# Optimization experiments

Hardware: AMD Instinct MI355X
Metric: run time of the kernel (lower is better)

The kernel has to match this reference:

```python
import jax, jax.numpy as jnp
import numpy as np

B, S, E, H = 2, 2048, 1024, 16
D = E // H  # head_dim = 64


def setup_inputs() -> dict:
    key = jax.random.key(0)
    ks = jax.random.split(key, 6)
    sc = 1.0 / np.sqrt(D)
    return {
        "x": jax.random.normal(ks[0], (B, S, E), dtype=jnp.float32),
        "Wq": jax.random.normal(ks[1], (D, D), dtype=jnp.float32) * sc,
        "Wk": jax.random.normal(ks[2], (D, D), dtype=jnp.float32) * sc,
        "Wv": jax.random.normal(ks[3], (D, D), dtype=jnp.float32) * sc,
        "Wo": jax.random.normal(ks[4], (E, E), dtype=jnp.float32) * (1.0 / np.sqrt(E)),
        "bo": jnp.zeros((E,), dtype=jnp.float32),
    }


def reference(x, Wq, Wk, Wv, Wo, bo):
    b, s, e = x.shape
    # split into heads: (B, H, S, D)
    xh = x.reshape(b, s, H, D).transpose(0, 2, 1, 3)
    # per-head linear projections (weights SHARED across heads); torch Linear: x @ W^T
    q = jnp.einsum('bhsd,ed->bhse', xh, Wq)
    k = jnp.einsum('bhsd,ed->bhse', xh, Wk)
    v = jnp.einsum('bhsd,ed->bhse', xh, Wv)
    # full attention matrix (B, H, S, S) — faithful to the naive original
    energy = jnp.einsum('bhqd,bhkd->bhqk', q, k)
    attn = jax.nn.softmax(energy / jnp.sqrt(jnp.asarray(D, x.dtype)), axis=-1)
    out = jnp.einsum('bhqk,bhkd->bhqd', attn, v)
    out = out.transpose(0, 2, 1, 3).reshape(b, s, e)
    return out @ Wo.T + bo
```

## Files before the change

### kernel.cpp

```cpp
#include <hip/hip_runtime.h>
#include <hip/hip_bf16.h>

#define B 2
#define S 2048
#define E 1024
#define H 16
#define D 64

typedef unsigned short ushort_t;
typedef __attribute__((ext_vector_type(8))) short bf16x8;
typedef __attribute__((ext_vector_type(4))) float f32x4;
typedef __attribute__((ext_vector_type(16))) float f32x16;

static __device__ __forceinline__ ushort_t f2bf(float f) {
    union { float f; unsigned u; } v; v.f = f;
    unsigned r = v.u + 0x7fffu + ((v.u >> 16) & 1u);
    return (ushort_t)(r >> 16);
}

#define MFMA(a, b, c)   __builtin_amdgcn_mfma_f32_16x16x32_bf16((a), (b), (c), 0, 0, 0)
#define MFMA32(a, b, c) __builtin_amdgcn_mfma_f32_32x32x16_bf16((a), (b), (c), 0, 0, 0)
#define PACKBF(hi, lo) __builtin_amdgcn_perm((hi), (lo), 0x07060302u)
#define LBAR() do { asm volatile("s_waitcnt lgkmcnt(0)" ::: "memory"); \
                    __builtin_amdgcn_s_barrier(); } while (0)

__global__ __launch_bounds__(256) void qkv_proj(
    const float* __restrict__ x,
    const float* __restrict__ Wq, const float* __restrict__ Wk, const float* __restrict__ Wv,
    const float* __restrict__ Wo,
    ushort_t* __restrict__ q, ushort_t* __restrict__ k, ushort_t* __restrict__ vT,
    ushort_t* __restrict__ wob)
{
    __shared__ ushort_t Xs[64][72];
    __shared__ ushort_t Wqs[64][72], Wks[64][72], Wvs[64][72];
    int t = threadIdx.x;
    int bh = blockIdx.y, b = bh >> 4, h = bh & 15;
    int s0 = blockIdx.x * 64;

    {
        int woid = blockIdx.y * 32 + blockIdx.x;
        int i = woid * 1024 + t * 4;
        float4 f = *(const float4*)(Wo + i);
        ushort4 u2; u2.x = f2bf(f.x); u2.y = f2bf(f.y); u2.z = f2bf(f.z); u2.w = f2bf(f.w);
        *(ushort4*)(wob + i) = u2;
    }
    {
        int i = t >> 2, d0 = (t & 3) * 16;
        const float* xp = x + ((size_t)(b * S + s0 + i)) * E + h * D + d0;
        #pragma unroll
        for (int c = 0; c < 16; c += 4) {
            float4 f = *(const float4*)(xp + c);
            Xs[i][d0 + c + 0] = f2bf(f.x); Xs[i][d0 + c + 1] = f2bf(f.y);
            Xs[i][d0 + c + 2] = f2bf(f.z); Xs[i][d0 + c + 3] = f2bf(f.w);
        }
    }
    {
        int e = t >> 2, d0 = (t & 3) * 16;
        const float* wqp = Wq + e * 64 + d0;
        const float* wkp = Wk + e * 64 + d0;
        const float* wvp = Wv + e * 64 + d0;
        #pragma unroll
        for (int c = 0; c < 16; c += 4) {
            float4 fq = *(const float4*)(wqp + c);
            Wqs[e][d0 + c + 0] = f2bf(fq.x * 0.18033688011112042f);
            Wqs[e][d0 + c + 1] = f2bf(fq.y * 0.18033688011112042f);
            Wqs[e][d0 + c + 2] = f2bf(fq.z * 0.18033688011112042f);
            Wqs[e][d0 + c + 3] = f2bf(fq.w * 0.18033688011112042f);
            float4 fk = *(const float4*)(wkp + c);
            Wks[e][d0 + c + 0] = f2bf(fk.x); Wks[e][d0 + c + 1] = f2bf(fk.y);
            Wks[e][d0 + c + 2] = f2bf(fk.z); Wks[e][d0 + c + 3] = f2bf(fk.w);
            float4 fv = *(const float4*)(wvp + c);
            Wvs[e][d0 + c + 0] = f2bf(fv.x); Wvs[e][d0 + c + 1] = f2bf(fv.y);
            Wvs[e][d0 + c + 2] = f2bf(fv.z); Wvs[e][d0 + c + 3] = f2bf(fv.w);
        }
    }
    __syncthreads();

    int w = t >> 6, lane = t & 63, m = lane & 15, quad = lane >> 4;
    bf16x8 a0 = *(bf16x8*)&Xs[16 * w + m][quad * 8];
    bf16x8 a1 = *(bf16x8*)&Xs[16 * w + m][32 + quad * 8];
    f32x4 cq[4], ck[4], cv[4];
    #pragma unroll
    for (int nt = 0; nt < 4; nt++) { cq[nt] = (f32x4)0.f; ck[nt] = (f32x4)0.f; cv[nt] = (f32x4)0.f; }
    #pragma unroll
    for (int nt = 0; nt < 4; nt++) {
        bf16x8 b0, b1;
        b0 = *(bf16x8*)&Wqs[nt * 16 + m][quad * 8]; b1 = *(bf16x8*)&Wqs[nt * 16 + m][32 + quad * 8];
        cq[nt] = MFMA(a0, b0, cq[nt]); cq[nt] = MFMA(a1, b1, cq[nt]);
        b0 = *(bf16x8*)&Wks[nt * 16 + m][quad * 8]; b1 = *(bf16x8*)&Wks[nt * 16 + m][32 + quad * 8];
        ck[nt] = MFMA(a0, b0, ck[nt]); ck[nt] = MFMA(a1, b1, ck[nt]);
        b0 = *(bf16x8*)&Wvs[nt * 16 + m][quad * 8]; b1 = *(bf16x8*)&Wvs[nt * 16 + m][32 + quad * 8];
        cv[nt] = MFMA(a0, b0, cv[nt]); cv[nt] = MFMA(a1, b1, cv[nt]);
    }
    size_t base = (size_t)bh * S + s0;
    #pragma unroll
    for (int nt = 0; nt < 4; nt++)
        #pragma unroll
        for (int r = 0; r < 4; r++) {
            size_t idx = (base + 16 * w + quad * 4 + r) * D + nt * 16 + m;
            q[idx] = f2bf(cq[nt][r]);
            k[idx] = f2bf(ck[nt][r]);
        }
    __syncthreads();
    #pragma unroll
    for (int nt = 0; nt < 4; nt++)
        #pragma unroll
        for (int r = 0; r < 4; r++)
            Wvs[nt * 16 + m][16 * w + quad * 4 + r] = f2bf(cv[nt][r]);
    __syncthreads();
    {
        int d0 = t >> 2, sc = (t & 3) * 16;
        ushort_t* vp = vT + ((size_t)bh * D + d0) * S + s0 + sc;
        *(bf16x8*)(vp)     = *(bf16x8*)&Wvs[d0][sc];
        *(bf16x8*)(vp + 8) = *(bf16x8*)&Wvs[d0][sc + 8];
    }
}

__global__ __launch_bounds__(512, 4) void flash_attn(
    const ushort_t* __restrict__ q, const ushort_t* __restrict__ k,
    const ushort_t* __restrict__ vT, ushort_t* __restrict__ ao)
{
    __shared__ ushort_t Ks[2][2][64][72];
    __shared__ ushort_t Vt[2][2][64][72];
    int t = threadIdx.x;
    int lin = blockIdx.x;
    int xcd = lin & 7, loc = lin >> 3;
    int bh = xcd * 4 + (loc >> 4);
    int q0 = (loc & 15) * 128;
    int b = bh >> 4, h = bh & 15;
    int w = t >> 6, lane = t & 63, l31 = lane & 31, half = lane >> 5;
    int g = w >> 2, wq = w & 3;
    int tg = t & 255;

    const ushort_t* qb = q + ((size_t)bh * S + q0) * D;
    const ushort_t* kb = k + (size_t)bh * S * D;
    const ushort_t* vb = vT + (size_t)bh * D * S;

    bf16x8 qf[4];
    {
        const ushort_t* qp = qb + (size_t)(wq * 32 + l31) * D + half * 8;
        #pragma unroll
        for (int c = 0; c < 4; c++) qf[c] = *(const bf16x8*)(qp + c * 16);
    }

    f32x16 o0 = (f32x16)0.f, o1 = (f32x16)0.f;
    float2 ls2 = make_float2(0.f, 0.f);

    int sr = tg >> 2, scc = (tg & 3) * 16;
    bf16x8 kp0, kp1, vp0, vp1;

    {
        int k00 = g * 64;
        const ushort_t* kp = kb + (size_t)(k00 + sr) * D + scc;
        const ushort_t* vp = vb + (size_t)sr * S + k00 + scc;
        kp0 = *(const bf16x8*)(kp);     kp1 = *(const bf16x8*)(kp + 8);
        vp0 = *(const bf16x8*)(vp);     vp1 = *(const bf16x8*)(vp + 8);
        *(bf16x8*)&Ks[g][0][sr][scc]     = kp0;
        *(bf16x8*)&Ks[g][0][sr][scc + 8] = kp1;
        *(bf16x8*)&Vt[g][0][sr][scc]     = vp0;
        *(bf16x8*)&Vt[g][0][sr][scc + 8] = vp1;
    }
    LBAR();
    {
        int k01 = (2 + g) * 64;
        const ushort_t* kp = kb + (size_t)(k01 + sr) * D + scc;
        const ushort_t* vp = vb + (size_t)sr * S + k01 + scc;
        kp0 = *(const bf16x8*)(kp);     kp1 = *(const bf16x8*)(kp + 8);
        vp0 = *(const bf16x8*)(vp);     vp1 = *(const bf16x8*)(vp + 8);
    }

    const int NJ = S / 128;
    for (int jt = 0; jt < NJ; jt++) {
        int p = jt & 1;
        if (jt + 1 < NJ) {
            *(bf16x8*)&Ks[g][1 - p][sr][scc]     = kp0;
            *(bf16x8*)&Ks[g][1 - p][sr][scc + 8] = kp1;
            *(bf16x8*)&Vt[g][1 - p][sr][scc]     = vp0;
            *(bf16x8*)&Vt[g][1 - p][sr][scc + 8] = vp1;
        }
        if (jt + 2 < NJ) {
            int k0n = (2 * (jt + 2) + g) * 64;
            const ushort_t* kp = kb + (size_t)(k0n + sr) * D + scc;
            const ushort_t* vp = vb + (size_t)sr * S + k0n + scc;
            kp0 = *(const bf16x8*)(kp);     kp1 = *(const bf16x8*)(kp + 8);
            vp0 = *(const bf16x8*)(vp);     vp1 = *(const bf16x8*)(vp + 8);
        }

        union { unsigned u[4]; bf16x8 v; } pa[4];
        #pragma unroll
        for (int st = 0; st < 2; st++) {
            f32x16 e = (f32x16)0.f;
            __builtin_amdgcn_s_setprio(1);
            #pragma unroll
            for (int c = 0; c < 4; c++) {
                bf16x8 ka = *(bf16x8*)&Ks[g][p][st * 32 + l31][c * 16 + half * 8];
                e = MFMA32(ka, qf[c], e);
            }
            __builtin_amdgcn_s_setprio(0);
            unsigned pt[16];
            #pragma unroll
            for (int r = 0; r < 16; r += 2) {
                float pe0 = __builtin_amdgcn_exp2f(e[r]);
                float pe1 = __builtin_amdgcn_exp2f(e[r + 1]);
                ls2.x += pe0; ls2.y += pe1;
                pt[r]     = __float_as_uint(pe0);
                pt[r + 1] = __float_as_uint(pe1);
            }
            #pragma unroll
            for (int c2 = 0; c2 < 2; c2++) {
                int rb = c2 * 8;
                unsigned dA = PACKBF(pt[rb + 1], pt[rb + 0]);
                unsigned dB = PACKBF(pt[rb + 3], pt[rb + 2]);
                unsigned dC = PACKBF(pt[rb + 5], pt[rb + 4]);
                unsigned dD = PACKBF(pt[rb + 7], pt[rb + 6]);
                asm volatile("v_permlane32_swap_b32 %0, %1" : "+v"(dA), "+v"(dC));
                asm volatile("v_permlane32_swap_b32 %0, %1" : "+v"(dB), "+v"(dD));
                int kc = st * 2 + c2;
                pa[kc].u[0] = dA;
                pa[kc].u[1] = dB;
                pa[kc].u[2] = dC;
                pa[kc].u[3] = dD;
            }
        }

        __builtin_amdgcn_s_setprio(1);
        #pragma unroll
        for (int kc = 0; kc < 4; kc++) {
            bf16x8 vf0 = *(bf16x8*)&Vt[g][p][l31][kc * 16 + half * 8];
            bf16x8 vf1 = *(bf16x8*)&Vt[g][p][32 + l31][kc * 16 + half * 8];
            o0 = MFMA32(pa[kc].v, vf0, o0);
            o1 = MFMA32(pa[kc].v, vf1, o1);
        }
        __builtin_amdgcn_s_setprio(0);
        LBAR();
    }

    float lsum = ls2.x + ls2.y;
    float* cmb = (float*)&Ks[0][0][0][0];
    int slot = (wq * 64 + lane) * 33;
    if (g == 1) {
        #pragma unroll
        for (int r2 = 0; r2 < 16; r2++) { cmb[slot + r2] = o0[r2]; cmb[slot + 16 + r2] = o1[r2]; }
        cmb[slot + 32] = lsum;
    }
    __syncthreads();
    if (g == 0) {
        #pragma unroll
        for (int r2 = 0; r2 < 16; r2++) { o0[r2] += cmb[slot + r2]; o1[r2] += cmb[slot + 16 + r2]; }
        lsum += cmb[slot + 32];
        float lfull = lsum + __shfl_xor(lsum, 32, 64);
        float inv = 1.001953125f / lfull;
        #pragma unroll
        for (int reg = 0; reg < 16; reg++) {
            int qrow = (reg & 3) + 8 * (reg >> 2) + 4 * half;
            float li = __shfl(inv, qrow, 64);
            int srow = q0 + wq * 32 + qrow;
            size_t base2 = ((size_t)(b * S + srow)) * E + h * D + l31;
            ao[base2]      = f2bf(o0[reg] * li);
            ao[base2 + 32] = f2bf(o1[reg] * li);
        }
    }
}

__global__ __launch_bounds__(512) void out_proj(
    const ushort_t* __restrict__ A, const ushort_t* __restrict__ Wob,
    const float* __restrict__ bo, float* __restrict__ Y)
{
    __shared__ ushort_t As[2][128][72];
    __shared__ ushort_t Ws[2][64][72];
    int t = threadIdx.x;
    int hwb = blockIdx.x;
    int swz = (hwb & 7) * 64 + (hwb >> 3);
    int n0 = (swz & 15) * 64, m0 = (swz >> 4) * 128;
    int w = t >> 6, lane = t & 63, m = lane & 15, quad = lane >> 4;
    f32x4 acc[4];
    #pragma unroll
    for (int nt = 0; nt < 4; nt++) acc[nt] = (f32x4)0.f;

    int ar = t >> 2, ac = (t & 3) * 16;
    int wr = t >> 3, wc = (t & 7) * 8;
    const ushort_t* apb = A + (size_t)(m0 + ar) * E + ac;
    const ushort_t* wpb = Wob + (size_t)(n0 + wr) * E + wc;

    bf16x8 arg[2], wrg;
    {
        *(bf16x8*)&As[0][ar][ac]     = *(const bf16x8*)(apb);
        *(bf16x8*)&As[0][ar][ac + 8] = *(const bf16x8*)(apb + 8);
        *(bf16x8*)&Ws[0][wr][wc]     = *(const bf16x8*)(wpb);
    }
    LBAR();
    {
        arg[0] = *(const bf16x8*)(apb + 64);
        arg[1] = *(const bf16x8*)(apb + 64 + 8);
        wrg    = *(const bf16x8*)(wpb + 64);
    }

    const int KT = E / 64;
    for (int ks = 0; ks < KT; ks++) {
        int p = ks & 1;
        if (ks + 1 < KT) {
            *(bf16x8*)&As[1 - p][ar][ac]     = arg[0];
            *(bf16x8*)&As[1 - p][ar][ac + 8] = arg[1];
            *(bf16x8*)&Ws[1 - p][wr][wc]     = wrg;
        }
        if (ks + 2 < KT) {
            int off = (ks + 2) * 64;
            arg[0] = *(const bf16x8*)(apb + off);
            arg[1] = *(const bf16x8*)(apb + off + 8);
            wrg    = *(const bf16x8*)(wpb + off);
        }
        #pragma unroll
        for (int h2 = 0; h2 < 2; h2++) {
            bf16x8 af = *(bf16x8*)&As[p][w * 16 + m][h2 * 32 + quad * 8];
            #pragma unroll
            for (int nt = 0; nt < 4; nt++) {
                bf16x8 bfr = *(bf16x8*)&Ws[p][nt * 16 + m][h2 * 32 + quad * 8];
                acc[nt] = MFMA(af, bfr, acc[nt]);
            }
        }
        LBAR();
    }
    #pragma unroll
    for (int nt = 0; nt < 4; nt++)
        #pragma unroll
        for (int r = 0; r < 4; r++) {
            int row = m0 + w * 16 + quad * 4 + r;
            int col = n0 + nt * 16 + m;
            Y[(size_t)row * E + col] = acc[nt][r] + bo[col];
        }
}

extern "C" void kernel_launch(void* const* d_in, const int* in_sizes, int n_in,
                              void* d_out, int out_size, void* d_ws, size_t ws_size,
                              hipStream_t stream)
{
    const float* x  = (const float*)d_in[0];
    const float* Wq = (const float*)d_in[1];
    const float* Wk = (const float*)d_in[2];
    const float* Wv = (const float*)d_in[3];
    const float* Wo = (const float*)d_in[4];
    const float* bo = (const float*)d_in[5];
    float* Y = (float*)d_out;

    const size_t n = (size_t)B * H * S * D;
    ushort_t* qw  = (ushort_t*)d_ws;
    ushort_t* kw  = qw + n;
    ushort_t* vTw = kw + n;
    ushort_t* ao  = vTw + n;
    ushort_t* wob = ao + n;

    qkv_proj<<<dim3(S / 64, B * H), 256, 0, stream>>>(x, Wq, Wk, Wv, Wo, qw, kw, vTw, wob);
    flash_attn<<<dim3((S / 128) * B * H), 512, 0, stream>>>(qw, kw, vTw, ao);
    out_proj<<<dim3(512), 512, 0, stream>>>(ao, wob, bo, Y);
}
```

Baseline: 141.8 us.

## Fuse projection, attention and output GEMM into one cooperative kernel with grid syncs

Merges the three kernels (QKV projection, flash attention, output projection) into a single cooperative persistent kernel of 512 blocks. The phases are separated by grid.sync and reuse one shared-memory buffer. The aim is to remove the launch gaps and tails between kernels. In exchange, the QKV phase now uses 512-thread blocks, each covering two 64-row halves, and the kernel depends on every block being co-resident (512 blocks at 4 per CU). If the cooperative launch fails, it falls back to the original three launches.

```diff
diff --git a/kernel.cpp b/kernel.cpp
--- a/kernel.cpp
+++ b/kernel.cpp
@@ -1,5 +1,8 @@
 #include <hip/hip_runtime.h>
 #include <hip/hip_bf16.h>
+#include <hip/hip_cooperative_groups.h>
+
+namespace cg = cooperative_groups;
 
 #define B 2
 #define S 2048
@@ -21,8 +24,317 @@
 #define MFMA(a, b, c)   __builtin_amdgcn_mfma_f32_16x16x32_bf16((a), (b), (c), 0, 0, 0)
 #define MFMA32(a, b, c) __builtin_amdgcn_mfma_f32_32x32x16_bf16((a), (b), (c), 0, 0, 0)
 #define PACKBF(hi, lo) __builtin_amdgcn_perm((hi), (lo), 0x07060302u)
+#define WQSCALE 0.18033688011112042f
 #define LBAR() do { asm volatile("s_waitcnt lgkmcnt(0)" ::: "memory"); \
                     __builtin_amdgcn_s_barrier(); } while (0)
+
+__global__ __launch_bounds__(512, 4) void fused_all(
+    const float* __restrict__ x,
+    const float* __restrict__ Wq, const float* __restrict__ Wk, const float* __restrict__ Wv,
+    const float* __restrict__ Wo, const float* __restrict__ bo,
+    ushort_t* __restrict__ q, ushort_t* __restrict__ k, ushort_t* __restrict__ vT,
+    ushort_t* __restrict__ ao, ushort_t* __restrict__ wob, float* __restrict__ Y)
+{
+    __shared__ char smem[73728];
+    cg::grid_group grid = cg::this_grid();
+    int th = threadIdx.x;
+    int lin = blockIdx.x;
+    int xcd = lin & 7, loc = lin >> 3;
+    int bh = xcd * 4 + (loc >> 4);
+    int b = bh >> 4, h = bh & 15;
+
+    {
+        ushort_t (*Xs)[64][72] = (ushort_t (*)[64][72])smem;
+        ushort_t (*Wqs)[72] = (ushort_t (*)[72])(smem + 18432);
+        ushort_t (*Wks)[72] = (ushort_t (*)[72])(smem + 27648);
+        ushort_t (*Wvs)[72] = (ushort_t (*)[72])(smem + 36864);
+        int hhalf = th >> 8, t = th & 255;
+        int s0 = (loc & 15) * 128 + hhalf * 64;
+
+        {
+            int i = lin * 2048 + th * 4;
+            float4 f = *(const float4*)(Wo + i);
+            ushort4 u2; u2.x = f2bf(f.x); u2.y = f2bf(f.y); u2.z = f2bf(f.z); u2.w = f2bf(f.w);
+            *(ushort4*)(wob + i) = u2;
+        }
+        {
+            int i = t >> 2, d0 = (t & 3) * 16;
+            const float* xp = x + ((size_t)(b * S + s0 + i)) * E + h * D + d0;
+            #pragma unroll
+            for (int c = 0; c < 16; c += 4) {
+                float4 f = *(const float4*)(xp + c);
+                Xs[hhalf][i][d0 + c + 0] = f2bf(f.x); Xs[hhalf][i][d0 + c + 1] = f2bf(f.y);
+                Xs[hhalf][i][d0 + c + 2] = f2bf(f.z); Xs[hhalf][i][d0 + c + 3] = f2bf(f.w);
+            }
+        }
+        {
+            int rw = th >> 3, c8 = (th & 7) * 8;
+            const float* wqp = Wq + rw * 64 + c8;
+            const float* wkp = Wk + rw * 64 + c8;
+            const float* wvp = Wv + rw * 64 + c8;
+            float4 f0 = *(const float4*)(wqp), f1 = *(const float4*)(wqp + 4);
+            Wqs[rw][c8 + 0] = f2bf(f0.x * WQSCALE); Wqs[rw][c8 + 1] = f2bf(f0.y * WQSCALE);
+            Wqs[rw][c8 + 2] = f2bf(f0.z * WQSCALE); Wqs[rw][c8 + 3] = f2bf(f0.w * WQSCALE);
+            Wqs[rw][c8 + 4] = f2bf(f1.x * WQSCALE); Wqs[rw][c8 + 5] = f2bf(f1.y * WQSCALE);
+            Wqs[rw][c8 + 6] = f2bf(f1.z * WQSCALE); Wqs[rw][c8 + 7] = f2bf(f1.w * WQSCALE);
+            f0 = *(const float4*)(wkp); f1 = *(const float4*)(wkp + 4);
+            Wks[rw][c8 + 0] = f2bf(f0.x); Wks[rw][c8 + 1] = f2bf(f0.y);
+            Wks[rw][c8 + 2] = f2bf(f0.z); Wks[rw][c8 + 3] = f2bf(f0.w);
+            Wks[rw][c8 + 4] = f2bf(f1.x); Wks[rw][c8 + 5] = f2bf(f1.y);
+            Wks[rw][c8 + 6] = f2bf(f1.z); Wks[rw][c8 + 7] = f2bf(f1.w);
+            f0 = *(const float4*)(wvp); f1 = *(const float4*)(wvp + 4);
+            Wvs[rw][c8 + 0] = f2bf(f0.x); Wvs[rw][c8 + 1] = f2bf(f0.y);
+            Wvs[rw][c8 + 2] = f2bf(f0.z); Wvs[rw][c8 + 3] = f2bf(f0.w);
+            Wvs[rw][c8 + 4] = f2bf(f1.x); Wvs[rw][c8 + 5] = f2bf(f1.y);
+            Wvs[rw][c8 + 6] = f2bf(f1.z); Wvs[rw][c8 + 7] = f2bf(f1.w);
+        }
+        __syncthreads();
+
+        int w = (th >> 6) & 3, lane = th & 63, m = lane & 15, quad = lane >> 4;
+        bf16x8 a0 = *(bf16x8*)&Xs[hhalf][16 * w + m][quad * 8];
+        bf16x8 a1 = *(bf16x8*)&Xs[hhalf][16 * w + m][32 + quad * 8];
+        f32x4 cq[4], ck[4], cv[4];
+        #pragma unroll
+        for (int nt = 0; nt < 4; nt++) { cq[nt] = (f32x4)0.f; ck[nt] = (f32x4)0.f; cv[nt] = (f32x4)0.f; }
+        #pragma unroll
+        for (int nt = 0; nt < 4; nt++) {
+            bf16x8 b0, b1;
+            b0 = *(bf16x8*)&Wqs[nt * 16 + m][quad * 8]; b1 = *(bf16x8*)&Wqs[nt * 16 + m][32 + quad * 8];
+            cq[nt] = MFMA(a0, b0, cq[nt]); cq[nt] = MFMA(a1, b1, cq[nt]);
+            b0 = *(bf16x8*)&Wks[nt * 16 + m][quad * 8]; b1 = *(bf16x8*)&Wks[nt * 16 + m][32 + quad * 8];
+            ck[nt] = MFMA(a0, b0, ck[nt]); ck[nt] = MFMA(a1, b1, ck[nt]);
+            b0 = *(bf16x8*)&Wvs[nt * 16 + m][quad * 8]; b1 = *(bf16x8*)&Wvs[nt * 16 + m][32 + quad * 8];
+            cv[nt] = MFMA(a0, b0, cv[nt]); cv[nt] = MFMA(a1, b1, cv[nt]);
+        }
+        size_t base = (size_t)bh * S + s0;
+        #pragma unroll
+        for (int nt = 0; nt < 4; nt++)
+            #pragma unroll
+            for (int r = 0; r < 4; r++) {
+                size_t idx = (base + 16 * w + quad * 4 + r) * D + nt * 16 + m;
+                q[idx] = f2bf(cq[nt][r]);
+                k[idx] = f2bf(ck[nt][r]);
+            }
+        __syncthreads();
+        #pragma unroll
+        for (int nt = 0; nt < 4; nt++)
+            #pragma unroll
+            for (int r = 0; r < 4; r++)
+                Xs[hhalf][nt * 16 + m][16 * w + quad * 4 + r] = f2bf(cv[nt][r]);
+        __syncthreads();
+        {
+            int d0 = t >> 2, sc = (t & 3) * 16;
+            ushort_t* vp = vT + ((size_t)bh * D + d0) * S + s0 + sc;
+            *(bf16x8*)(vp)     = *(bf16x8*)&Xs[hhalf][d0][sc];
+            *(bf16x8*)(vp + 8) = *(bf16x8*)&Xs[hhalf][d0][sc + 8];
+        }
+    }
+    grid.sync();
+
+    {
+        ushort_t (*Ks)[2][64][72] = (ushort_t (*)[2][64][72])smem;
+        ushort_t (*Vt)[2][64][72] = (ushort_t (*)[2][64][72])(smem + 36864);
+        int t = th;
+        int q0 = (loc & 15) * 128;
+        int w = t >> 6, lane = t & 63, l31 = lane & 31, half = lane >> 5;
+        int g = w >> 2, wqw = w & 3;
+        int tg = t & 255;
+
+        const ushort_t* qb = q + ((size_t)bh * S + q0) * D;
+        const ushort_t* kb = k + (size_t)bh * S * D;
+        const ushort_t* vb = vT + (size_t)bh * D * S;
+
+        bf16x8 qf[4];
+        {
+            const ushort_t* qp = qb + (size_t)(wqw * 32 + l31) * D + half * 8;
+            #pragma unroll
+            for (int c = 0; c < 4; c++) qf[c] = *(const bf16x8*)(qp + c * 16);
+        }
+
+        f32x16 o0 = (f32x16)0.f, o1 = (f32x16)0.f;
+        float2 ls2 = make_float2(0.f, 0.f);
+
+        int sr = tg >> 2, scc = (tg & 3) * 16;
+        bf16x8 kp0, kp1, vp0, vp1;
+
+        {
+            int k00 = g * 64;
+            const ushort_t* kp = kb + (size_t)(k00 + sr) * D + scc;
+            const ushort_t* vp = vb + (size_t)sr * S + k00 + scc;
+            kp0 = *(const bf16x8*)(kp);     kp1 = *(const bf16x8*)(kp + 8);
+            vp0 = *(const bf16x8*)(vp);     vp1 = *(const bf16x8*)(vp + 8);
+            *(bf16x8*)&Ks[g][0][sr][scc]     = kp0;
+            *(bf16x8*)&Ks[g][0][sr][scc + 8] = kp1;
+            *(bf16x8*)&Vt[g][0][sr][scc]     = vp0;
+            *(bf16x8*)&Vt[g][0][sr][scc + 8] = vp1;
+        }
+        LBAR();
+        {
+            int k01 = (2 + g) * 64;
+            const ushort_t* kp = kb + (size_t)(k01 + sr) * D + scc;
+            const ushort_t* vp = vb + (size_t)sr * S + k01 + scc;
+            kp0 = *(const bf16x8*)(kp);     kp1 = *(const bf16x8*)(kp + 8);
+            vp0 = *(const bf16x8*)(vp);     vp1 = *(const bf16x8*)(vp + 8);
+        }
+
+        const int NJ = S / 128;
+        for (int jt = 0; jt < NJ; jt++) {
+            int p = jt & 1;
+            if (jt + 1 < NJ) {
+                *(bf16x8*)&Ks[g][1 - p][sr][scc]     = kp0;
+                *(bf16x8*)&Ks[g][1 - p][sr][scc + 8] = kp1;
+                *(bf16x8*)&Vt[g][1 - p][sr][scc]     = vp0;
+                *(bf16x8*)&Vt[g][1 - p][sr][scc + 8] = vp1;
+            }
+            if (jt + 2 < NJ) {
+                int k0n = (2 * (jt + 2) + g) * 64;
+                const ushort_t* kp = kb + (size_t)(k0n + sr) * D + scc;
+                const ushort_t* vp = vb + (size_t)sr * S + k0n + scc;
+                kp0 = *(const bf16x8*)(kp);     kp1 = *(const bf16x8*)(kp + 8);
+                vp0 = *(const bf16x8*)(vp);     vp1 = *(const bf16x8*)(vp + 8);
+            }
+
+            union { unsigned u[4]; bf16x8 v; } pa[4];
+            #pragma unroll
+            for (int st = 0; st < 2; st++) {
+                f32x16 e = (f32x16)0.f;
+                __builtin_amdgcn_s_setprio(1);
+                #pragma unroll
+                for (int c = 0; c < 4; c++) {
+                    bf16x8 ka = *(bf16x8*)&Ks[g][p][st * 32 + l31][c * 16 + half * 8];
+                    e = MFMA32(ka, qf[c], e);
+                }
+                __builtin_amdgcn_s_setprio(0);
+                unsigned pt[16];
+                #pragma unroll
+                for (int r = 0; r < 16; r += 2) {
+                    float pe0 = __builtin_amdgcn_exp2f(e[r]);
+                    float pe1 = __builtin_amdgcn_exp2f(e[r + 1]);
+                    ls2.x += pe0; ls2.y += pe1;
+                    pt[r]     = __float_as_uint(pe0);
+                    pt[r + 1] = __float_as_uint(pe1);
+                }
+                #pragma unroll
+                for (int c2 = 0; c2 < 2; c2++) {
+                    int rb = c2 * 8;
+                    unsigned dA = PACKBF(pt[rb + 1], pt[rb + 0]);
+                    unsigned dB = PACKBF(pt[rb + 3], pt[rb + 2]);
+                    unsigned dC = PACKBF(pt[rb + 5], pt[rb + 4]);
+                    unsigned dD = PACKBF(pt[rb + 7], pt[rb + 6]);
+                    asm volatile("v_permlane32_swap_b32 %0, %1" : "+v"(dA), "+v"(dC));
+                    asm volatile("v_permlane32_swap_b32 %0, %1" : "+v"(dB), "+v"(dD));
+                    int kc = st * 2 + c2;
+                    pa[kc].u[0] = dA;
+                    pa[kc].u[1] = dB;
+                    pa[kc].u[2] = dC;
+                    pa[kc].u[3] = dD;
+                }
+            }
+
+            __builtin_amdgcn_s_setprio(1);
+            #pragma unroll
+            for (int kc = 0; kc < 4; kc++) {
+                bf16x8 vf0 = *(bf16x8*)&Vt[g][p][l31][kc * 16 + half * 8];
+                bf16x8 vf1 = *(bf16x8*)&Vt[g][p][32 + l31][kc * 16 + half * 8];
+                o0 = MFMA32(pa[kc].v, vf0, o0);
+                o1 = MFMA32(pa[kc].v, vf1, o1);
+            }
+            __builtin_amdgcn_s_setprio(0);
+            LBAR();
+        }
+
+        float lsum = ls2.x + ls2.y;
+        float* cmb = (float*)smem;
+        int slot = (wqw * 64 + lane) * 33;
+        if (g == 1) {
+            #pragma unroll
+            for (int r2 = 0; r2 < 16; r2++) { cmb[slot + r2] = o0[r2]; cmb[slot + 16 + r2] = o1[r2]; }
+            cmb[slot + 32] = lsum;
+        }
+        __syncthreads();
+        if (g == 0) {
+            #pragma unroll
+            for (int r2 = 0; r2 < 16; r2++) { o0[r2] += cmb[slot + r2]; o1[r2] += cmb[slot + 16 + r2]; }
+            lsum += cmb[slot + 32];
+            float lfull = lsum + __shfl_xor(lsum, 32, 64);
+            float inv = 1.001953125f / lfull;
+            #pragma unroll
+            for (int reg = 0; reg < 16; reg++) {
+                int qrow = (reg & 3) + 8 * (reg >> 2) + 4 * half;
+                float li = __shfl(inv, qrow, 64);
+                int srow = q0 + wqw * 32 + qrow;
+                size_t base2 = ((size_t)(b * S + srow)) * E + h * D + l31;
+                ao[base2]      = f2bf(o0[reg] * li);
+                ao[base2 + 32] = f2bf(o1[reg] * li);
+            }
+        }
+    }
+    grid.sync();
+
+    {
+        ushort_t (*As)[128][72] = (ushort_t (*)[128][72])smem;
+        ushort_t (*Ws)[64][72]  = (ushort_t (*)[64][72])(smem + 36864);
+        int t = th;
+        int swz = (lin & 7) * 64 + (lin >> 3);
+        int n0 = (swz & 15) * 64, m0 = (swz >> 4) * 128;
+        int w = t >> 6, lane = t & 63, m = lane & 15, quad = lane >> 4;
+        f32x4 acc[4];
+        #pragma unroll
+        for (int nt = 0; nt < 4; nt++) acc[nt] = (f32x4)0.f;
+
+        int ar = t >> 2, ac = (t & 3) * 16;
+        int wr = t >> 3, wc = (t & 7) * 8;
+        const ushort_t* apb = ao + (size_t)(m0 + ar) * E + ac;
+        const ushort_t* wpb = wob + (size_t)(n0 + wr) * E + wc;
+
+        bf16x8 arg[2], wrg;
+        {
+            *(bf16x8*)&As[0][ar][ac]     = *(const bf16x8*)(apb);
+            *(bf16x8*)&As[0][ar][ac + 8] = *(const bf16x8*)(apb + 8);
+            *(bf16x8*)&Ws[0][wr][wc]     = *(const bf16x8*)(wpb);
+        }
+        LBAR();
+        {
+            arg[0] = *(const bf16x8*)(apb + 64);
+            arg[1] = *(const bf16x8*)(apb + 64 + 8);
+            wrg    = *(const bf16x8*)(wpb + 64);
+        }
+
+        const int KT = E / 64;
+        for (int ks = 0; ks < KT; ks++) {
+            int p = ks & 1;
+            if (ks + 1 < KT) {
+                *(bf16x8*)&As[1 - p][ar][ac]     = arg[0];
+                *(bf16x8*)&As[1 - p][ar][ac + 8] = arg[1];
+                *(bf16x8*)&Ws[1 - p][wr][wc]     = wrg;
+            }
+            if (ks + 2 < KT) {
+                int off = (ks + 2) * 64;
+                arg[0] = *(const bf16x8*)(apb + off);
+                arg[1] = *(const bf16x8*)(apb + off + 8);
+                wrg    = *(const bf16x8*)(wpb + off);
+            }
+            #pragma unroll
+            for (int h2 = 0; h2 < 2; h2++) {
+                bf16x8 af = *(bf16x8*)&As[p][w * 16 + m][h2 * 32 + quad * 8];
+                #pragma unroll
+                for (int nt = 0; nt < 4; nt++) {
+                    bf16x8 bfr = *(bf16x8*)&Ws[p][nt * 16 + m][h2 * 32 + quad * 8];
+                    acc[nt] = MFMA(af, bfr, acc[nt]);
+                }
+            }
+            LBAR();
+        }
+        #pragma unroll
+        for (int nt = 0; nt < 4; nt++)
+            #pragma unroll
+            for (int r = 0; r < 4; r++) {
+                int row = m0 + w * 16 + quad * 4 + r;
+                int col = n0 + nt * 16 + m;
+                Y[(size_t)row * E + col] = acc[nt][r] + bo[col];
+            }
+    }
+}
 
 __global__ __launch_bounds__(256) void qkv_proj(
     const float* __restrict__ x,
@@ -36,7 +348,6 @@
     int t = threadIdx.x;
     int bh = blockIdx.y, b = bh >> 4, h = bh & 15;
     int s0 = blockIdx.x * 64;
-
     {
         int woid = blockIdx.y * 32 + blockIdx.x;
         int i = woid * 1024 + t * 4;
@@ -62,10 +373,10 @@
         #pragma unroll
         for (int c = 0; c < 16; c += 4) {
             float4 fq = *(const float4*)(wqp + c);
-            Wqs[e][d0 + c + 0] = f2bf(fq.x * 0.18033688011112042f);
-            Wqs[e][d0 + c + 1] = f2bf(fq.y * 0.18033688011112042f);
-            Wqs[e][d0 + c + 2] = f2bf(fq.z * 0.18033688011112042f);
-            Wqs[e][d0 + c + 3] = f2bf(fq.w * 0.18033688011112042f);
+            Wqs[e][d0 + c + 0] = f2bf(fq.x * WQSCALE);
+            Wqs[e][d0 + c + 1] = f2bf(fq.y * WQSCALE);
+            Wqs[e][d0 + c + 2] = f2bf(fq.z * WQSCALE);
+            Wqs[e][d0 + c + 3] = f2bf(fq.w * WQSCALE);
             float4 fk = *(const float4*)(wkp + c);
             Wks[e][d0 + c + 0] = f2bf(fk.x); Wks[e][d0 + c + 1] = f2bf(fk.y);
             Wks[e][d0 + c + 2] = f2bf(fk.z); Wks[e][d0 + c + 3] = f2bf(fk.w);
@@ -75,7 +386,6 @@
         }
     }
     __syncthreads();
-
     int w = t >> 6, lane = t & 63, m = lane & 15, quad = lane >> 4;
     bf16x8 a0 = *(bf16x8*)&Xs[16 * w + m][quad * 8];
     bf16x8 a1 = *(bf16x8*)&Xs[16 * w + m][32 + quad * 8];
@@ -129,7 +439,7 @@
     int q0 = (loc & 15) * 128;
     int b = bh >> 4, h = bh & 15;
     int w = t >> 6, lane = t & 63, l31 = lane & 31, half = lane >> 5;
-    int g = w >> 2, wq = w & 3;
+    int g = w >> 2, wqw = w & 3;
     int tg = t & 255;
 
     const ushort_t* qb = q + ((size_t)bh * S + q0) * D;
@@ -138,17 +448,14 @@
 
     bf16x8 qf[4];
     {
-        const ushort_t* qp = qb + (size_t)(wq * 32 + l31) * D + half * 8;
+        const ushort_t* qp = qb + (size_t)(wqw * 32 + l31) * D + half * 8;
         #pragma unroll
         for (int c = 0; c < 4; c++) qf[c] = *(const bf16x8*)(qp + c * 16);
     }
-
     f32x16 o0 = (f32x16)0.f, o1 = (f32x16)0.f;
     float2 ls2 = make_float2(0.f, 0.f);
-
     int sr = tg >> 2, scc = (tg & 3) * 16;
     bf16x8 kp0, kp1, vp0, vp1;
-
     {
         int k00 = g * 64;
         const ushort_t* kp = kb + (size_t)(k00 + sr) * D + scc;
@@ -168,7 +475,6 @@
         kp0 = *(const bf16x8*)(kp);     kp1 = *(const bf16x8*)(kp + 8);
         vp0 = *(const bf16x8*)(vp);     vp1 = *(const bf16x8*)(vp + 8);
     }
-
     const int NJ = S / 128;
     for (int jt = 0; jt < NJ; jt++) {
         int p = jt & 1;
@@ -185,7 +491,6 @@
             kp0 = *(const bf16x8*)(kp);     kp1 = *(const bf16x8*)(kp + 8);
             vp0 = *(const bf16x8*)(vp);     vp1 = *(const bf16x8*)(vp + 8);
         }
-
         union { unsigned u[4]; bf16x8 v; } pa[4];
         #pragma unroll
         for (int st = 0; st < 2; st++) {
@@ -222,7 +527,6 @@
                 pa[kc].u[3] = dD;
             }
         }
-
         __builtin_amdgcn_s_setprio(1);
         #pragma unroll
         for (int kc = 0; kc < 4; kc++) {
@@ -234,10 +538,9 @@
         __builtin_amdgcn_s_setprio(0);
         LBAR();
     }
-
     float lsum = ls2.x + ls2.y;
     float* cmb = (float*)&Ks[0][0][0][0];
-    int slot = (wq * 64 + lane) * 33;
+    int slot = (wqw * 64 + lane) * 33;
     if (g == 1) {
         #pragma unroll
         for (int r2 = 0; r2 < 16; r2++) { cmb[slot + r2] = o0[r2]; cmb[slot + 16 + r2] = o1[r2]; }
@@ -254,7 +557,7 @@
         for (int reg = 0; reg < 16; reg++) {
             int qrow = (reg & 3) + 8 * (reg >> 2) + 4 * half;
             float li = __shfl(inv, qrow, 64);
-            int srow = q0 + wq * 32 + qrow;
+            int srow = q0 + wqw * 32 + qrow;
             size_t base2 = ((size_t)(b * S + srow)) * E + h * D + l31;
             ao[base2]      = f2bf(o0[reg] * li);
             ao[base2 + 32] = f2bf(o1[reg] * li);
@@ -276,12 +579,10 @@
     f32x4 acc[4];
     #pragma unroll
     for (int nt = 0; nt < 4; nt++) acc[nt] = (f32x4)0.f;
-
     int ar = t >> 2, ac = (t & 3) * 16;
     int wr = t >> 3, wc = (t & 7) * 8;
     const ushort_t* apb = A + (size_t)(m0 + ar) * E + ac;
     const ushort_t* wpb = Wob + (size_t)(n0 + wr) * E + wc;
-
     bf16x8 arg[2], wrg;
     {
         *(bf16x8*)&As[0][ar][ac]     = *(const bf16x8*)(apb);
@@ -294,7 +595,6 @@
         arg[1] = *(const bf16x8*)(apb + 64 + 8);
         wrg    = *(const bf16x8*)(wpb + 64);
     }
-
     const int KT = E / 64;
     for (int ks = 0; ks < KT; ks++) {
         int p = ks & 1;
@@ -349,7 +649,15 @@
     ushort_t* ao  = vTw + n;
     ushort_t* wob = ao + n;
 
-    qkv_proj<<<dim3(S / 64, B * H), 256, 0, stream>>>(x, Wq, Wk, Wv, Wo, qw, kw, vTw, wob);
-    flash_attn<<<dim3((S / 128) * B * H), 512, 0, stream>>>(qw, kw, vTw, ao);
-    out_proj<<<dim3(512), 512, 0, stream>>>(ao, wob, bo, Y);
+    void* kargs[] = {
+        (void*)&x, (void*)&Wq, (void*)&Wk, (void*)&Wv, (void*)&Wo, (void*)&bo,
+        (void*)&qw, (void*)&kw, (void*)&vTw, (void*)&ao, (void*)&wob, (void*)&Y
+    };
+    hipError_t err = hipLaunchCooperativeKernel((void*)fused_all, dim3(512), dim3(512),
+                                                kargs, 0, stream);
+    if (err != hipSuccess) {
+        qkv_proj<<<dim3(S / 64, B * H), 256, 0, stream>>>(x, Wq, Wk, Wv, Wo, qw, kw, vTw, wob);
+        flash_attn<<<dim3((S / 128) * B * H), 512, 0, stream>>>(qw, kw, vTw, ao);
+        out_proj<<<dim3(512), 512, 0, stream>>>(ao, wob, bo, Y);
+    }
 }
```

Result: slower. 289.7 us (+104.2%).
